# Performance work log

Measured on AMD Instinct MI355X. Metric: run time of the kernel, lower is better.

## Reference

```python
import jax, jax.numpy as jnp
import numpy as np

HIDDEN = 4096


def setup_inputs() -> dict:
    key = jax.random.key(0)
    k1, k2 = jax.random.split(key)
    hidden_states = jax.random.normal(k1, (8, 2048, HIDDEN), dtype=jnp.float32)
    # gate_proj ~ N(0, 0.02^2), shape (2*hidden, hidden)
    gate_proj = 0.02 * jax.random.normal(k2, (2 * HIDDEN, HIDDEN), dtype=jnp.float32)
    return {"hidden_states": hidden_states, "gate_proj": gate_proj, "world_size": 8}


def reference(hidden_states, gate_proj, world_size):
    h = gate_proj.shape[1]
    view = hidden_states.reshape(-1, h)                 # [N, h]
    mm = jnp.einsum("nh,oh->no", view, gate_proj)      # [N, 2h]  (x @ W.T)
    n, o = mm.shape
    # reduce-scatter over dim 0 with world_size ranks: sum the per-rank chunks
    out = mm.reshape(world_size, n // world_size, o).sum(axis=0)  # [N/W, 2h]
    return out
```

## Files before the change

### kernel.cpp

```cpp
#include <hip/hip_runtime.h>
#include <hip/hip_bf16.h>


#define HID   4096
#define SEQ   2048
#define WORLD 8
#define OUTD  8192

typedef __bf16 bf16x8 __attribute__((ext_vector_type(8)));
typedef short  s16x8  __attribute__((ext_vector_type(8)));
typedef float  f32x4  __attribute__((ext_vector_type(4)));

typedef const __attribute__((address_space(1))) void* gas1_ptr;
typedef __attribute__((address_space(3))) void*       las3_ptr;

static __device__ __forceinline__ unsigned short f2bf(float f) {
    union { float f; unsigned u; } v; v.f = f;
    unsigned u = v.u;
    u += 0x7fffu + ((u >> 16) & 1u);
    return (unsigned short)(u >> 16);
}

#define RED_BLOCKS  2048
#define CONV_BLOCKS 4096
__global__ void prep_kernel(const float* __restrict__ hs,
                            const float* __restrict__ w,
                            unsigned short* __restrict__ xb,
                            unsigned short* __restrict__ wb) {
    if (blockIdx.x < RED_BLOCKS) {
        const int total4 = SEQ * HID / 4;
        const float4* h4 = (const float4*)hs;
        ushort4* o4 = (ushort4*)xb;
        for (int i = blockIdx.x * blockDim.x + threadIdx.x; i < total4;
             i += RED_BLOCKS * blockDim.x) {
            float4 s = h4[i];
            #pragma unroll
            for (int ww = 1; ww < WORLD; ++ww) {
                float4 t = h4[i + ww * total4];
                s.x += t.x; s.y += t.y; s.z += t.z; s.w += t.w;
            }
            ushort4 o;
            o.x = f2bf(s.x); o.y = f2bf(s.y); o.z = f2bf(s.z); o.w = f2bf(s.w);
            o4[i] = o;
        }
    } else {
        const int total4 = OUTD * HID / 4;
        const float4* w4 = (const float4*)w;
        ushort4* o4 = (ushort4*)wb;
        for (int i = (blockIdx.x - RED_BLOCKS) * blockDim.x + threadIdx.x;
             i < total4; i += CONV_BLOCKS * blockDim.x) {
            float4 s = w4[i];
            ushort4 o;
            o.x = f2bf(s.x); o.y = f2bf(s.y); o.z = f2bf(s.z); o.w = f2bf(s.w);
            o4[i] = o;
        }
    }
}


#define BM 256
#define BN 256
#define BK 64
#define KSTEPS (HID / BK)

__global__ __launch_bounds__(512, 2)
void gemm_bt_kernel(const unsigned short* __restrict__ A,
                    const unsigned short* __restrict__ B,
                    float* __restrict__ C) {
    __shared__ __align__(16) unsigned short lsA[2][BM * BK];
    __shared__ __align__(16) unsigned short lsB[2][BN * BK];

    const int tid  = threadIdx.x;
    const int lane = tid & 63;
    const int wave = tid >> 6;
    const int wm   = wave >> 2;
    const int wn   = wave & 3;

    const int bid   = blockIdx.x;
    const int xcd   = bid & 7;
    const int local = bid >> 3;
    const int bm = (xcd >> 2) * 4 + (local >> 3);
    const int bn = (xcd & 3) * 8 + (local & 7);

    const int subrow = lane >> 3;
    const int slot   = lane & 7;
    const int scol   = (slot ^ subrow) * 8;
    const unsigned short* aBase =
        A + (size_t)(bm * BM + wave * 8 + subrow) * HID + scol;
    const unsigned short* bBase =
        B + (size_t)(bn * BN + wave * 8 + subrow) * HID + scol;
    const int ldsW = wave * 8 * BK;

#define ST_A(buf, ktv, l) __builtin_amdgcn_global_load_lds(                     \
        (gas1_ptr)(aBase + (size_t)(ktv) * BK + (size_t)(l) * 64 * HID),        \
        (las3_ptr)(&lsA[buf][(l) * 64 * BK + ldsW]), 16, 0, 0)
#define ST_B(buf, ktv, l) __builtin_amdgcn_global_load_lds(                     \
        (gas1_ptr)(bBase + (size_t)(ktv) * BK + (size_t)(l) * 64 * HID),        \
        (las3_ptr)(&lsB[buf][(l) * 64 * BK + ldsW]), 16, 0, 0)
#define STG_A(buf, ktv, h) do { ST_A(buf, ktv, 2*(h)); ST_A(buf, ktv, 2*(h)+1); } while (0)
#define STG_B(buf, ktv, h) do { ST_B(buf, ktv, 2*(h)); ST_B(buf, ktv, 2*(h)+1); } while (0)

    const int fr    = lane & 15;
    const int fq    = lane >> 4;
    const int axor  = fr & 7;
    const int koff0 = ((0 + fq) ^ axor) * 8;
    const int koff1 = ((4 + fq) ^ axor) * 8;
    const int aRowB = (wm * 128 + fr) * BK;
    const int bRowB = (wn * 64 + fr) * BK;

#define RD_A(dst, P, mm, koff) dst = __builtin_bit_cast(bf16x8,                 \
        *(const s16x8*)&lsA[P][aRowB + (mm) * 16 * BK + (koff)])
#define RD_B(dst, P, nn, koff) dst = __builtin_bit_cast(bf16x8,                 \
        *(const s16x8*)&lsB[P][bRowB + (nn) * 16 * BK + (koff)])

#define BARRIER() __builtin_amdgcn_s_barrier()
#define LGKM0()   asm volatile("s_waitcnt lgkmcnt(0)" ::: "memory")
#define LGKM8()   asm volatile("s_waitcnt lgkmcnt(8)" ::: "memory")
#define VMC6()    asm volatile("s_waitcnt vmcnt(6)" ::: "memory")
#define VMC0()    asm volatile("s_waitcnt vmcnt(0)" ::: "memory")
#define PRIO1()   __builtin_amdgcn_s_setprio(1)
#define PRIO0()   __builtin_amdgcn_s_setprio(0)

#define MFMA16(VAx, mb)                                                          \
    PRIO1();                                                                     \
    _Pragma("unroll")                                                            \
    for (int s = 0; s < 2; ++s)                                                  \
        _Pragma("unroll")                                                        \
        for (int m = 0; m < 2; ++m)                                              \
            _Pragma("unroll")                                                    \
            for (int n = 0; n < 4; ++n)                                          \
                acc[(mb) + m][n] = __builtin_amdgcn_mfma_f32_16x16x32_bf16(      \
                    VAx[m][s], vb[n][s], acc[(mb) + m][n], 0, 0, 0);             \
    PRIO0()

#define READS_PH_FIRST(P)                                                        \
    RD_B(vb[0][0], P, 0, koff0); RD_B(vb[0][1], P, 0, koff1);                    \
    RD_B(vb[1][0], P, 1, koff0); RD_B(vb[1][1], P, 1, koff1);                    \
    RD_B(vb[2][0], P, 2, koff0); RD_B(vb[2][1], P, 2, koff1);                    \
    RD_B(vb[3][0], P, 3, koff0); RD_B(vb[3][1], P, 3, koff1);                    \
    RD_A(va[0][0], P, 0, koff0); RD_A(va[0][1], P, 0, koff1);                    \
    RD_A(va[1][0], P, 1, koff0); RD_A(va[1][1], P, 1, koff1)

    f32x4 acc[8][4] = {};
    bf16x8 va[2][2], va2[2][2], vb[4][2];

    STG_B(0, 0, 0); STG_B(0, 0, 1); STG_A(0, 0, 0); STG_A(0, 0, 1);
    STG_B(1, 1, 0); STG_B(1, 1, 1); STG_A(1, 1, 0);
    VMC6();
    BARRIER();

    #pragma unroll 1
    for (int t = 0; t < KSTEPS; t += 2) {
        const bool st2 = (t + 2 < KSTEPS);
        const bool st3 = (t + 3 < KSTEPS);

        READS_PH_FIRST(0);
        STG_A(1, t + 1, 1);
        LGKM8();
        BARRIER(); LGKM0();
        MFMA16(va, 0);
        BARRIER();

        RD_A(va[0][0], 0, 2, koff0); RD_A(va[0][1], 0, 2, koff1);
        RD_A(va[1][0], 0, 3, koff0); RD_A(va[1][1], 0, 3, koff1);
        if (st2) STG_B(0, t + 2, 0);
        BARRIER(); LGKM0();
        MFMA16(va, 2);
        BARRIER();

        RD_A(va[0][0],  0, 4, koff0); RD_A(va[0][1],  0, 4, koff1);
        RD_A(va[1][0],  0, 5, koff0); RD_A(va[1][1],  0, 5, koff1);
        RD_A(va2[0][0], 0, 6, koff0); RD_A(va2[0][1], 0, 6, koff1);
        RD_A(va2[1][0], 0, 7, koff0); RD_A(va2[1][1], 0, 7, koff1);
        if (st2) STG_B(0, t + 2, 1);
        BARRIER(); LGKM0();
        MFMA16(va, 4);
        BARRIER();

        if (st2) STG_A(0, t + 2, 0);
        BARRIER();
        MFMA16(va2, 6);
        if (st2) { VMC6(); } else { VMC0(); }
        BARRIER();

        READS_PH_FIRST(1);
        if (st2) STG_A(0, t + 2, 1);
        LGKM8();
        BARRIER(); LGKM0();
        MFMA16(va, 0);
        BARRIER();

        RD_A(va[0][0], 1, 2, koff0); RD_A(va[0][1], 1, 2, koff1);
        RD_A(va[1][0], 1, 3, koff0); RD_A(va[1][1], 1, 3, koff1);
        if (st3) STG_B(1, t + 3, 0);
        BARRIER(); LGKM0();
        MFMA16(va, 2);
        BARRIER();

        RD_A(va[0][0],  1, 4, koff0); RD_A(va[0][1],  1, 4, koff1);
        RD_A(va[1][0],  1, 5, koff0); RD_A(va[1][1],  1, 5, koff1);
        RD_A(va2[0][0], 1, 6, koff0); RD_A(va2[0][1], 1, 6, koff1);
        RD_A(va2[1][0], 1, 7, koff0); RD_A(va2[1][1], 1, 7, koff1);
        if (st3) STG_B(1, t + 3, 1);
        BARRIER(); LGKM0();
        MFMA16(va, 4);
        BARRIER();

        if (st3) STG_A(1, t + 3, 0);
        BARRIER();
        MFMA16(va2, 6);
        if (st3) { VMC6(); } else { VMC0(); }
        BARRIER();
    }

    const long crow0 = (long)bm * BM + wm * 128 + fq * 4;
    const long ccol0 = (long)bn * BN + wn * 64 + fr;
    #pragma unroll
    for (int m = 0; m < 8; ++m)
        #pragma unroll
        for (int n = 0; n < 4; ++n)
            #pragma unroll
            for (int j = 0; j < 4; ++j)
                C[(crow0 + m * 16 + j) * OUTD + ccol0 + n * 16] = acc[m][n][j];
}

extern "C" void kernel_launch(void* const* d_in, const int* in_sizes, int n_in,
                              void* d_out, int out_size, void* d_ws, size_t ws_size,
                              hipStream_t stream) {
    const float* hs = (const float*)d_in[0];
    const float* w  = (const float*)d_in[1];
    float* out = (float*)d_out;

    unsigned short* xb = (unsigned short*)d_ws;
    unsigned short* wb = xb + (size_t)SEQ * HID;

    hipLaunchKernelGGL(prep_kernel, dim3(RED_BLOCKS + CONV_BLOCKS), dim3(256),
                       0, stream, hs, w, xb, wb);
    hipLaunchKernelGGL(gemm_bt_kernel, dim3((SEQ / BM) * (OUTD / BN)), dim3(512),
                       0, stream, xb, wb, out);
}
```

Before: 223.0 us.

## Restructure GEMM main loop into barrier-light sections with batched prefetch

Replaces the fine-grained per-phase schedule, which used many barriers and LDS waits per k-step, with a section that issues LDS reads for the next A fragments while MFMAs on the previous ones run. Global-to-LDS staging for the next tile is issued in one batch after a single barrier, followed by a vmcnt(8) wait. This cuts the number of barriers per k-step from about eight to two, so waves stall less at synchronisation points. In exchange, global loads are less spread across the compute phases, and the implicit reliance on the compiler to insert lgkm waits before the MFMAs could affect correctness or the schedule.

```diff
diff --git a/kernel.cpp b/kernel.cpp
--- a/kernel.cpp
+++ b/kernel.cpp
@@ -115,8 +115,7 @@
 
 #define BARRIER() __builtin_amdgcn_s_barrier()
 #define LGKM0()   asm volatile("s_waitcnt lgkmcnt(0)" ::: "memory")
-#define LGKM8()   asm volatile("s_waitcnt lgkmcnt(8)" ::: "memory")
-#define VMC6()    asm volatile("s_waitcnt vmcnt(6)" ::: "memory")
+#define VMC8()    asm volatile("s_waitcnt vmcnt(8)" ::: "memory")
 #define VMC0()    asm volatile("s_waitcnt vmcnt(0)" ::: "memory")
 #define PRIO1()   __builtin_amdgcn_s_setprio(1)
 #define PRIO0()   __builtin_amdgcn_s_setprio(0)
@@ -133,84 +132,44 @@
                     VAx[m][s], vb[n][s], acc[(mb) + m][n], 0, 0, 0);             \
     PRIO0()
 
-#define READS_PH_FIRST(P)                                                        \
+#define TILE_SECTION(P, Tnext, ST)                                               \
     RD_B(vb[0][0], P, 0, koff0); RD_B(vb[0][1], P, 0, koff1);                    \
     RD_B(vb[1][0], P, 1, koff0); RD_B(vb[1][1], P, 1, koff1);                    \
     RD_B(vb[2][0], P, 2, koff0); RD_B(vb[2][1], P, 2, koff1);                    \
     RD_B(vb[3][0], P, 3, koff0); RD_B(vb[3][1], P, 3, koff1);                    \
     RD_A(va[0][0], P, 0, koff0); RD_A(va[0][1], P, 0, koff1);                    \
-    RD_A(va[1][0], P, 1, koff0); RD_A(va[1][1], P, 1, koff1)
+    RD_A(va[1][0], P, 1, koff0); RD_A(va[1][1], P, 1, koff1);                    \
+    RD_A(vc[0][0], P, 2, koff0); RD_A(vc[0][1], P, 2, koff1);                    \
+    RD_A(vc[1][0], P, 3, koff0); RD_A(vc[1][1], P, 3, koff1);                    \
+    MFMA16(va, 0);                                                               \
+    RD_A(va[0][0], P, 4, koff0); RD_A(va[0][1], P, 4, koff1);                    \
+    RD_A(va[1][0], P, 5, koff0); RD_A(va[1][1], P, 5, koff1);                    \
+    MFMA16(vc, 2);                                                               \
+    RD_A(vc[0][0], P, 6, koff0); RD_A(vc[0][1], P, 6, koff1);                    \
+    RD_A(vc[1][0], P, 7, koff0); RD_A(vc[1][1], P, 7, koff1);                    \
+    MFMA16(va, 4);                                                               \
+    LGKM0();                                                                     \
+    BARRIER();                                                                   \
+    if (ST) { STG_A(P, Tnext, 0); STG_A(P, Tnext, 1);                            \
+              STG_B(P, Tnext, 0); STG_B(P, Tnext, 1); }                          \
+    MFMA16(vc, 6);                                                               \
+    if (ST) { VMC8(); } else { VMC0(); }                                         \
+    BARRIER()
 
     f32x4 acc[8][4] = {};
-    bf16x8 va[2][2], va2[2][2], vb[4][2];
-
-    STG_B(0, 0, 0); STG_B(0, 0, 1); STG_A(0, 0, 0); STG_A(0, 0, 1);
-    STG_B(1, 1, 0); STG_B(1, 1, 1); STG_A(1, 1, 0);
-    VMC6();
+    bf16x8 va[2][2], vc[2][2], vb[4][2];
+
+    STG_A(0, 0, 0); STG_A(0, 0, 1); STG_B(0, 0, 0); STG_B(0, 0, 1);
+    STG_A(1, 1, 0); STG_A(1, 1, 1); STG_B(1, 1, 0); STG_B(1, 1, 1);
+    VMC8();
     BARRIER();
 
     #pragma unroll 1
     for (int t = 0; t < KSTEPS; t += 2) {
-        const bool st2 = (t + 2 < KSTEPS);
-        const bool st3 = (t + 3 < KSTEPS);
-
-        READS_PH_FIRST(0);
-        STG_A(1, t + 1, 1);
-        LGKM8();
-        BARRIER(); LGKM0();
-        MFMA16(va, 0);
-        BARRIER();
-
-        RD_A(va[0][0], 0, 2, koff0); RD_A(va[0][1], 0, 2, koff1);
-        RD_A(va[1][0], 0, 3, koff0); RD_A(va[1][1], 0, 3, koff1);
-        if (st2) STG_B(0, t + 2, 0);
-        BARRIER(); LGKM0();
-        MFMA16(va, 2);
-        BARRIER();
-
-        RD_A(va[0][0],  0, 4, koff0); RD_A(va[0][1],  0, 4, koff1);
-        RD_A(va[1][0],  0, 5, koff0); RD_A(va[1][1],  0, 5, koff1);
-        RD_A(va2[0][0], 0, 6, koff0); RD_A(va2[0][1], 0, 6, koff1);
-        RD_A(va2[1][0], 0, 7, koff0); RD_A(va2[1][1], 0, 7, koff1);
-        if (st2) STG_B(0, t + 2, 1);
-        BARRIER(); LGKM0();
-        MFMA16(va, 4);
-        BARRIER();
-
-        if (st2) STG_A(0, t + 2, 0);
-        BARRIER();
-        MFMA16(va2, 6);
-        if (st2) { VMC6(); } else { VMC0(); }
-        BARRIER();
-
-        READS_PH_FIRST(1);
-        if (st2) STG_A(0, t + 2, 1);
-        LGKM8();
-        BARRIER(); LGKM0();
-        MFMA16(va, 0);
-        BARRIER();
-
-        RD_A(va[0][0], 1, 2, koff0); RD_A(va[0][1], 1, 2, koff1);
-        RD_A(va[1][0], 1, 3, koff0); RD_A(va[1][1], 1, 3, koff1);
-        if (st3) STG_B(1, t + 3, 0);
-        BARRIER(); LGKM0();
-        MFMA16(va, 2);
-        BARRIER();
-
-        RD_A(va[0][0],  1, 4, koff0); RD_A(va[0][1],  1, 4, koff1);
-        RD_A(va[1][0],  1, 5, koff0); RD_A(va[1][1],  1, 5, koff1);
-        RD_A(va2[0][0], 1, 6, koff0); RD_A(va2[0][1], 1, 6, koff1);
-        RD_A(va2[1][0], 1, 7, koff0); RD_A(va2[1][1], 1, 7, koff1);
-        if (st3) STG_B(1, t + 3, 1);
-        BARRIER(); LGKM0();
-        MFMA16(va, 4);
-        BARRIER();
-
-        if (st3) STG_A(1, t + 3, 0);
-        BARRIER();
-        MFMA16(va2, 6);
-        if (st3) { VMC6(); } else { VMC0(); }
-        BARRIER();
+        const bool s2 = (t + 2 < KSTEPS);
+        const bool s3 = (t + 3 < KSTEPS);
+        TILE_SECTION(0, t + 2, s2);
+        TILE_SECTION(1, t + 3, s3);
     }
 
     const long crow0 = (long)bm * BM + wm * 128 + fq * 4;
```

Result: slower. 228.2 us (+2.3%).
